# Performance work log

Hardware: AMD Instinct MI355X
Metric: run time of the kernel (lower is better)

Reference implementation:

```python
import jax, jax.numpy as jnp
import numpy as np

N_NODES = 50000
N_EDGES = 800000
DIM = 128
N_LAYERS = 5
BN_EPS = 1e-3  # keras BatchNormalization default epsilon


def setup_inputs() -> dict:
    key = jax.random.key(0)
    ks = jax.random.split(key, 6)
    scale = 1.0 / np.sqrt(DIM)
    return {
        "x": jax.random.normal(ks[0], (N_NODES, DIM), dtype=jnp.float32),
        "edge_src": jax.random.randint(ks[1], (N_EDGES,), 0, N_NODES, dtype=jnp.int32),
        "edge_dst": jax.random.randint(ks[2], (N_EDGES,), 0, N_NODES, dtype=jnp.int32),
        "eps": jnp.zeros((N_LAYERS,), dtype=jnp.float32),
        "W1": jax.random.normal(ks[3], (N_LAYERS, DIM, DIM), dtype=jnp.float32) * scale,
        "b1": jnp.zeros((N_LAYERS, DIM), dtype=jnp.float32),
        "W2": jax.random.normal(ks[4], (N_LAYERS, DIM, DIM), dtype=jnp.float32) * scale,
        "b2": jnp.zeros((N_LAYERS, DIM), dtype=jnp.float32),
        "gamma": jnp.ones((N_LAYERS, DIM), dtype=jnp.float32),
        "beta": jnp.zeros((N_LAYERS, DIM), dtype=jnp.float32),
        "bn_mean": jnp.zeros((N_LAYERS, DIM), dtype=jnp.float32),
        "bn_var": jnp.ones((N_LAYERS, DIM), dtype=jnp.float32),
    }


def reference(x, edge_src, edge_dst, eps, W1, b1, W2, b2, gamma, beta, bn_mean, bn_var):
    n = x.shape[0]
    num_layers = W1.shape[0]
    hidden_rep = [x]
    h = x
    for l in range(num_layers):
        # sparse Adj @ h as gather + segment-sum (sum neighbor pooling)
        msgs = jnp.take(h, edge_src, axis=0)                       # [E, D]
        pooled = jax.ops.segment_sum(msgs, edge_dst, num_segments=n)  # [N, D]
        pooled = pooled + (1.0 + eps[l]) * h                        # GIN eps term
        # 2-layer MLP: Linear -> ReLU -> Linear
        z = jax.nn.relu(pooled @ W1[l] + b1[l])
        z = z @ W2[l] + b2[l]
        # BatchNorm (inference: moving statistics)
        z = gamma[l] * (z - bn_mean[l]) * jax.lax.rsqrt(bn_var[l] + BN_EPS) + beta[l]
        h = jax.nn.relu(z)
        hidden_rep.append(h)
    return tuple(hidden_rep)
```

## Files before the change

### kernel.cpp

```cpp
#include <hip/hip_runtime.h>
#include <hip/hip_bf16.h>

#define N_NODES 50000
#define N_EDGES 800000
#define DIM 128
#define N_LAYERS 5
#define BN_EPS 1e-3f

typedef __attribute__((ext_vector_type(8))) short bf16x8;
typedef __attribute__((ext_vector_type(4))) float f32x4;

__device__ __forceinline__ unsigned short f2bf(float f) {
    unsigned int v = __builtin_bit_cast(unsigned int, f);
    v += 0x7fffu + ((v >> 16) & 1u);
    return (unsigned short)(v >> 16);
}
__device__ __forceinline__ float bflo(unsigned int v) {
    return __builtin_bit_cast(float, v << 16);
}
__device__ __forceinline__ float bfhi(unsigned int v) {
    return __builtin_bit_cast(float, v & 0xffff0000u);
}


__global__ void init_zero_kernel(const float* __restrict__ x, float* __restrict__ out,
                                 unsigned short* __restrict__ hb, int* __restrict__ cnt) {
    int t = blockIdx.x * blockDim.x + threadIdx.x;
    if (t < (N_NODES * DIM) / 4) {
        f32x4 v = ((const f32x4*)x)[t];
        __builtin_nontemporal_store(v, (f32x4*)out + t);
        unsigned short u[4] = {f2bf(v.x), f2bf(v.y), f2bf(v.z), f2bf(v.w)};
        *(uint2*)(hb + t * 4) = *(uint2*)u;
    }
    int z = t - (N_NODES * DIM) / 4;
    if (z >= 0 && z < N_NODES) cnt[z] = 0;
}

__global__ void hist_kernel(const int* __restrict__ dst, int* __restrict__ cnt) {
    int e = blockIdx.x * blockDim.x + threadIdx.x;
    if (e < N_EDGES) atomicAdd(&cnt[dst[e]], 1);
}

__global__ __launch_bounds__(1024) void scan_kernel(const int* __restrict__ cnt,
                                                    int* __restrict__ row_start,
                                                    int* __restrict__ cursor) {
    __shared__ int wsum[16];
    __shared__ int s_carry;
    const int tid = threadIdx.x;
    const int lane = tid & 63, wave = tid >> 6;
    if (tid == 0) s_carry = 0;
    __syncthreads();
    for (int base = 0; base < N_NODES; base += 4096) {
        int i0 = base + tid * 4;
        int v[4];
#pragma unroll
        for (int j = 0; j < 4; j++) {
            int i = i0 + j;
            v[j] = (i < N_NODES) ? cnt[i] : 0;
        }
        int s = v[0] + v[1] + v[2] + v[3];
        int x = s;
#pragma unroll
        for (int off = 1; off < 64; off <<= 1) {
            int t = __shfl_up(x, off, 64);
            if (lane >= off) x += t;
        }
        if (lane == 63) wsum[wave] = x;
        __syncthreads();
        if (wave == 0) {
            int w = (lane < 16) ? wsum[lane] : 0;
#pragma unroll
            for (int off = 1; off < 16; off <<= 1) {
                int t = __shfl_up(w, off, 64);
                if (lane >= off) w += t;
            }
            if (lane < 16) wsum[lane] = w;
        }
        __syncthreads();
        int waveoff = (wave > 0) ? wsum[wave - 1] : 0;
        int carry = s_carry;
        int run = carry + waveoff + (x - s);
#pragma unroll
        for (int j = 0; j < 4; j++) {
            int i = i0 + j;
            if (i < N_NODES) { row_start[i] = run; cursor[i] = run; }
            run += v[j];
        }
        __syncthreads();
        if (tid == 1023) s_carry = carry + wsum[15];
        __syncthreads();
    }
    if (tid == 0) row_start[N_NODES] = s_carry;
}

__global__ void fill_kernel(const int* __restrict__ src, const int* __restrict__ dst,
                            int* __restrict__ cursor, int* __restrict__ col) {
    int e = blockIdx.x * blockDim.x + threadIdx.x;
    if (e < N_EDGES) {
        int d = dst[e];
        int pos = atomicAdd(&cursor[d], 1);
        col[pos] = src[e];
    }
}

__global__ void prep_kernel(const float* __restrict__ W1, const float* __restrict__ W2,
                            unsigned short* __restrict__ wp,
                            const float* __restrict__ gamma, const float* __restrict__ beta,
                            const float* __restrict__ mean, const float* __restrict__ var,
                            float* __restrict__ scale, float* __restrict__ shift) {
    int t = blockIdx.x * blockDim.x + threadIdx.x;
    if (t < N_LAYERS * 2 * 2048) {
        int mat = t >> 11;
        int r = t & 2047;
        int ks = r >> 9, nt = (r >> 6) & 7, lane = r & 63;
        int layer = mat >> 1;
        const float* W = ((mat & 1) ? W2 : W1) + layer * DIM * DIM;
        int n = nt * 16 + (lane & 15);
        int kb = ks * 32 + (lane >> 4) * 8;
        unsigned short u[8];
#pragma unroll
        for (int j = 0; j < 8; j++) u[j] = f2bf(W[(kb + j) * DIM + n]);
        *(uint4*)(wp + (size_t)mat * 16384 + ((ks * 8 + nt) * 64 + lane) * 8) = *(uint4*)u;
    }
    int i = t - N_LAYERS * 2 * 2048;
    if (i >= 0 && i < N_LAYERS * DIM) {
        float sc = gamma[i] * rsqrtf(var[i] + BN_EPS);
        scale[i] = sc;
        shift[i] = beta[i] - mean[i] * sc;
    }
}


__global__ __launch_bounds__(256) void pool_kernel(const unsigned short* __restrict__ hb,
                                                   const int* __restrict__ row_start,
                                                   const int* __restrict__ col,
                                                   const float* __restrict__ eps_l,
                                                   unsigned short* __restrict__ pooled_b) {
    const int wave = threadIdx.x >> 6, lane = threadIdx.x & 63;
    const int n = blockIdx.x * 4 + wave;
    if (n >= N_NODES) return;
    const float ev = 1.0f + eps_l[0];
    const int s0 = row_start[n], s1 = row_start[n + 1];
    const int c2 = lane * 2;

    unsigned int sv = *(const unsigned int*)(hb + n * DIM + c2);
    float a0 = ev * bflo(sv);
    float a1 = ev * bfhi(sv);

    for (int base = s0; base < s1; base += 64) {
        const int nn = (s1 - base < 64) ? (s1 - base) : 64;
        int ci = (base + lane < s1) ? col[base + lane] : 0;
        for (int j = 0; j < nn; j += 8) {
            int s[8];
            unsigned int v[8];
#pragma unroll
            for (int q = 0; q < 8; q++) s[q] = __shfl(ci, j + q, 64);
#pragma unroll
            for (int q = 0; q < 8; q++)
                v[q] = *(const unsigned int*)(hb + s[q] * DIM + c2);
#pragma unroll
            for (int q = 0; q < 8; q++) {
                if (j + q < nn) { a0 += bflo(v[q]); a1 += bfhi(v[q]); }
            }
        }
    }
    unsigned short u[2] = {f2bf(a0), f2bf(a1)};
    *(unsigned int*)(pooled_b + n * DIM + c2) = *(unsigned int*)u;
}

__global__ __launch_bounds__(256) void mlp_kernel(
    const unsigned short* __restrict__ pooled_b,
    const unsigned short* __restrict__ wp1,
    const unsigned short* __restrict__ wp2,
    const float* __restrict__ b1,
    const float* __restrict__ b2,
    const float* __restrict__ bnscale,
    const float* __restrict__ bnshift,
    float* __restrict__ h_out,
    unsigned short* __restrict__ hb_out) {
    __shared__ __align__(16) unsigned short zfrag[4][4][64][8];
    const int tid = threadIdx.x;
    const int wave = tid >> 6, lane = tid & 63;
    const int m0 = blockIdx.x * 64;
    const int colc = lane & 15;
    const int quad = lane >> 4;
    const int arow = m0 + wave * 16 + colc;
    const int arow_c = arow < N_NODES ? arow : N_NODES - 1;

    bf16x8 a[4];
#pragma unroll
    for (int ks = 0; ks < 4; ks++)
        a[ks] = *(const bf16x8*)(pooled_b + arow_c * DIM + ks * 32 + quad * 8);

    f32x4 acc[8];
#pragma unroll
    for (int nt = 0; nt < 8; nt++) {
        acc[nt] = (f32x4){0.f, 0.f, 0.f, 0.f};
#pragma unroll
        for (int ks = 0; ks < 4; ks++) {
            bf16x8 b = *(const bf16x8*)(wp1 + ((ks * 8 + nt) * 64 + lane) * 8);
            acc[nt] = __builtin_amdgcn_mfma_f32_16x16x32_bf16(a[ks], b, acc[nt], 0, 0, 0);
        }
    }

#pragma unroll
    for (int nt = 0; nt < 8; nt++) {
        int n = nt * 16 + colc;
        float bias = b1[n];
#pragma unroll
        for (int r = 0; r < 4; r++) {
            float v = acc[nt][r] + bias;
            v = v > 0.f ? v : 0.f;
            int row16 = quad * 4 + r;
            zfrag[wave][n >> 5][(((n >> 3) & 3) << 4) | row16][n & 7] = f2bf(v);
        }
    }

#pragma unroll
    for (int ks = 0; ks < 4; ks++) a[ks] = *(const bf16x8*)(&zfrag[wave][ks][lane][0]);

    f32x4 acc2[8];
#pragma unroll
    for (int nt = 0; nt < 8; nt++) {
        acc2[nt] = (f32x4){0.f, 0.f, 0.f, 0.f};
#pragma unroll
        for (int ks = 0; ks < 4; ks++) {
            bf16x8 b = *(const bf16x8*)(wp2 + ((ks * 8 + nt) * 64 + lane) * 8);
            acc2[nt] = __builtin_amdgcn_mfma_f32_16x16x32_bf16(a[ks], b, acc2[nt], 0, 0, 0);
        }
    }

#pragma unroll
    for (int nt = 0; nt < 8; nt++) {
        int n = nt * 16 + colc;
        float bias = b2[n];
        float sc = bnscale[n], sh = bnshift[n];
#pragma unroll
        for (int r = 0; r < 4; r++) {
            int row = m0 + wave * 16 + quad * 4 + r;
            if (row < N_NODES) {
                float z = acc2[nt][r] + bias;
                z = z * sc + sh;
                z = z > 0.f ? z : 0.f;
                __builtin_nontemporal_store(z, &h_out[row * DIM + n]);
                hb_out[row * DIM + n] = f2bf(z);
            }
        }
    }
}


extern "C" void kernel_launch(void* const* d_in, const int* in_sizes, int n_in,
                              void* d_out, int out_size, void* d_ws, size_t ws_size,
                              hipStream_t stream) {
    const float* x     = (const float*)d_in[0];
    const int* esrc    = (const int*)d_in[1];
    const int* edst    = (const int*)d_in[2];
    const float* eps   = (const float*)d_in[3];
    const float* W1    = (const float*)d_in[4];
    const float* b1    = (const float*)d_in[5];
    const float* W2    = (const float*)d_in[6];
    const float* b2    = (const float*)d_in[7];
    const float* gam   = (const float*)d_in[8];
    const float* bet   = (const float*)d_in[9];
    const float* bmean = (const float*)d_in[10];
    const float* bvar  = (const float*)d_in[11];
    float* out = (float*)d_out;

    char* ws = (char*)d_ws;
    unsigned short* hb0   = (unsigned short*)(ws);
    unsigned short* hb1   = (unsigned short*)(ws + 12800000);
    int*   col        = (int*)  (ws + 25600000);
    int*   row_start  = (int*)  (ws + 28800000);
    int*   cursor     = (int*)  (ws + 29000008);
    int*   cnt        = (int*)  (ws + 29200008);
    unsigned short* wpack = (unsigned short*)(ws + 29400008);
    float* bnscale    = (float*)(ws + 29727688);
    float* bnshift    = (float*)(ws + 29730248);
    unsigned short* pooled_b = (unsigned short*)(ws + 29735048);

    init_zero_kernel<<<((N_NODES * DIM) / 4 + N_NODES + 255) / 256, 256, 0, stream>>>(
        x, out, hb0, cnt);
    hist_kernel<<<(N_EDGES + 255) / 256, 256, 0, stream>>>(edst, cnt);
    scan_kernel<<<1, 1024, 0, stream>>>(cnt, row_start, cursor);
    fill_kernel<<<(N_EDGES + 255) / 256, 256, 0, stream>>>(esrc, edst, cursor, col);
    prep_kernel<<<(N_LAYERS * 2 * 2048 + N_LAYERS * DIM + 255) / 256, 256, 0, stream>>>(
        W1, W2, wpack, gam, bet, bmean, bvar, bnscale, bnshift);

    const int pool_blocks = (N_NODES + 3) / 4;
    const int mlp_blocks  = (N_NODES + 63) / 64;
    unsigned short* hbuf[2] = {hb0, hb1};
    for (int l = 0; l < N_LAYERS; l++) {
        float* h_next = out + (size_t)(l + 1) * N_NODES * DIM;
        pool_kernel<<<pool_blocks, 256, 0, stream>>>(hbuf[l & 1], row_start, col, eps + l,
                                                     pooled_b);
        mlp_kernel<<<mlp_blocks, 256, 0, stream>>>(
            pooled_b,
            wpack + (size_t)(l * 2) * 16384,
            wpack + (size_t)(l * 2 + 1) * 16384,
            b1 + l * DIM, b2 + l * DIM,
            bnscale + l * DIM, bnshift + l * DIM,
            h_next, hbuf[(l + 1) & 1]);
    }
}
```

Baseline: 575.3 us.

## Quantize node features to int8 with per-column scales for neighbor gather

Adds a per-layer quantization pass that converts bf16 features to int8 using per-column absmax scales, tracked via atomics in the MLP epilogue and an initial colmax kernel. The pooling kernel gathers 16-byte int8 chunks with 8 lanes per row, accumulates in integers, reduces across lane groups, and rescales before adding the self term. This halves gather traffic in the neighbor aggregation. In exchange it adds an extra quantization pass per layer and loses accuracy from 8-bit rounding.

```diff
diff --git a/kernel.cpp b/kernel.cpp
--- a/kernel.cpp
+++ b/kernel.cpp
@@ -6,9 +6,12 @@
 #define DIM 128
 #define N_LAYERS 5
 #define BN_EPS 1e-3f
+#define CMPAD 16
 
 typedef __attribute__((ext_vector_type(8))) short bf16x8;
 typedef __attribute__((ext_vector_type(4))) float f32x4;
+typedef __attribute__((ext_vector_type(4))) unsigned int u32x4;
+typedef __attribute__((ext_vector_type(2))) unsigned int u32x2;
 
 __device__ __forceinline__ unsigned short f2bf(float f) {
     unsigned int v = __builtin_bit_cast(unsigned int, f);
@@ -24,16 +27,43 @@
 
 
 __global__ void init_zero_kernel(const float* __restrict__ x, float* __restrict__ out,
-                                 unsigned short* __restrict__ hb, int* __restrict__ cnt) {
+                                 unsigned short* __restrict__ hb, int* __restrict__ cnt,
+                                 unsigned int* __restrict__ cmax) {
     int t = blockIdx.x * blockDim.x + threadIdx.x;
     if (t < (N_NODES * DIM) / 4) {
         f32x4 v = ((const f32x4*)x)[t];
         __builtin_nontemporal_store(v, (f32x4*)out + t);
         unsigned short u[4] = {f2bf(v.x), f2bf(v.y), f2bf(v.z), f2bf(v.w)};
-        *(uint2*)(hb + t * 4) = *(uint2*)u;
+        *(u32x2*)(hb + t * 4) = *(u32x2*)u;
     }
     int z = t - (N_NODES * DIM) / 4;
     if (z >= 0 && z < N_NODES) cnt[z] = 0;
+    int z2 = z - N_NODES;
+    if (z2 >= 0 && z2 < 2 * DIM * CMPAD) cmax[z2] = 0;
+}
+
+__global__ __launch_bounds__(256) void colmax0_kernel(const unsigned short* __restrict__ hb,
+                                                      unsigned int* __restrict__ cmax) {
+    __shared__ unsigned int cm[DIM];
+    const int tid = threadIdx.x;
+    if (tid < DIM) cm[tid] = 0;
+    __syncthreads();
+    const int total = N_NODES * DIM / 8;
+    const int stride = gridDim.x * blockDim.x;
+    float m[8] = {0.f, 0.f, 0.f, 0.f, 0.f, 0.f, 0.f, 0.f};
+    for (int e = blockIdx.x * blockDim.x + tid; e < total; e += stride) {
+        u32x4 v = *(const u32x4*)(hb + (size_t)e * 8);
+        m[0] = fmaxf(m[0], fabsf(bflo(v.x))); m[1] = fmaxf(m[1], fabsf(bfhi(v.x)));
+        m[2] = fmaxf(m[2], fabsf(bflo(v.y))); m[3] = fmaxf(m[3], fabsf(bfhi(v.y)));
+        m[4] = fmaxf(m[4], fabsf(bflo(v.z))); m[5] = fmaxf(m[5], fabsf(bfhi(v.z)));
+        m[6] = fmaxf(m[6], fabsf(bflo(v.w))); m[7] = fmaxf(m[7], fabsf(bfhi(v.w)));
+    }
+    const int cb = (tid & 15) * 8;
+#pragma unroll
+    for (int k = 0; k < 8; k++)
+        atomicMax(&cm[cb + k], __builtin_bit_cast(unsigned int, m[k]));
+    __syncthreads();
+    if (tid < DIM) atomicMax(&cmax[tid * CMPAD], cm[tid]);
 }
 
 __global__ void hist_kernel(const int* __restrict__ dst, int* __restrict__ cnt) {
@@ -120,7 +150,7 @@
         unsigned short u[8];
 #pragma unroll
         for (int j = 0; j < 8; j++) u[j] = f2bf(W[(kb + j) * DIM + n]);
-        *(uint4*)(wp + (size_t)mat * 16384 + ((ks * 8 + nt) * 64 + lane) * 8) = *(uint4*)u;
+        *(u32x4*)(wp + (size_t)mat * 16384 + ((ks * 8 + nt) * 64 + lane) * 8) = *(u32x4*)u;
     }
     int i = t - N_LAYERS * 2 * 2048;
     if (i >= 0 && i < N_LAYERS * DIM) {
@@ -131,41 +161,110 @@
 }
 
 
-__global__ __launch_bounds__(256) void pool_kernel(const unsigned short* __restrict__ hb,
+__global__ __launch_bounds__(256) void quant_kernel(const unsigned short* __restrict__ hb,
+                                                    const unsigned int* __restrict__ cmax_cur,
+                                                    unsigned int* __restrict__ cmax_next,
+                                                    signed char* __restrict__ q8) {
+    const int tid = blockIdx.x * blockDim.x + threadIdx.x;
+    if (blockIdx.x == 0 && threadIdx.x < DIM) cmax_next[threadIdx.x * CMPAD] = 0;
+    const int cb = (tid & 15) * 8;
+    float inv[8];
+#pragma unroll
+    for (int k = 0; k < 8; k++) {
+        float mx = __builtin_bit_cast(float, cmax_cur[(cb + k) * CMPAD]);
+        inv[k] = mx > 0.f ? 127.0f / mx : 0.f;
+    }
+    u32x4 v = *(const u32x4*)(hb + (size_t)tid * 8);
+    float f[8] = {bflo(v.x), bfhi(v.x), bflo(v.y), bfhi(v.y),
+                  bflo(v.z), bfhi(v.z), bflo(v.w), bfhi(v.w)};
+    unsigned int b[8];
+#pragma unroll
+    for (int k = 0; k < 8; k++) {
+        int q = (int)rintf(f[k] * inv[k]);
+        q = q > 127 ? 127 : (q < -127 ? -127 : q);
+        b[k] = (unsigned int)q & 255u;
+    }
+    u32x2 o;
+    o.x = b[0] | (b[1] << 8) | (b[2] << 16) | (b[3] << 24);
+    o.y = b[4] | (b[5] << 8) | (b[6] << 16) | (b[7] << 24);
+    __builtin_nontemporal_store(o, (u32x2*)(q8 + (size_t)tid * 8));
+}
+
+__device__ __forceinline__ void accq(int* a, unsigned int w, int k) {
+    a[k + 0] += (int)(w << 24) >> 24;
+    a[k + 1] += (int)(w << 16) >> 24;
+    a[k + 2] += (int)(w << 8) >> 24;
+    a[k + 3] += (int)w >> 24;
+}
+
+__global__ __launch_bounds__(256) void pool_kernel(const signed char* __restrict__ q8,
+                                                   const unsigned short* __restrict__ hb,
                                                    const int* __restrict__ row_start,
                                                    const int* __restrict__ col,
                                                    const float* __restrict__ eps_l,
+                                                   const unsigned int* __restrict__ cmax,
                                                    unsigned short* __restrict__ pooled_b) {
     const int wave = threadIdx.x >> 6, lane = threadIdx.x & 63;
-    const int n = blockIdx.x * 4 + wave;
-    if (n >= N_NODES) return;
-    const float ev = 1.0f + eps_l[0];
+    const int n = __builtin_amdgcn_readfirstlane(blockIdx.x * 4 + wave);
     const int s0 = row_start[n], s1 = row_start[n + 1];
-    const int c2 = lane * 2;
-
-    unsigned int sv = *(const unsigned int*)(hb + n * DIM + c2);
-    float a0 = ev * bflo(sv);
-    float a1 = ev * bfhi(sv);
+    const int g = lane >> 3;
+    const int t = lane & 7;
+
+    int acc[16] = {0, 0, 0, 0, 0, 0, 0, 0, 0, 0, 0, 0, 0, 0, 0, 0};
 
     for (int base = s0; base < s1; base += 64) {
-        const int nn = (s1 - base < 64) ? (s1 - base) : 64;
-        int ci = (base + lane < s1) ? col[base + lane] : 0;
-        for (int j = 0; j < nn; j += 8) {
-            int s[8];
-            unsigned int v[8];
-#pragma unroll
-            for (int q = 0; q < 8; q++) s[q] = __shfl(ci, j + q, 64);
-#pragma unroll
-            for (int q = 0; q < 8; q++)
-                v[q] = *(const unsigned int*)(hb + s[q] * DIM + c2);
-#pragma unroll
-            for (int q = 0; q < 8; q++) {
-                if (j + q < nn) { a0 += bflo(v[q]); a1 += bfhi(v[q]); }
+        const int rem = s1 - base;
+        const int nn = rem < 64 ? rem : 64;
+        int ci = (base + lane < s1) ? __builtin_nontemporal_load(&col[base + lane]) : 0;
+        for (int j = 0; j < nn; j += 24) {
+            u32x4 v[3];
+#pragma unroll
+            for (int i = 0; i < 3; i++) {
+                int start = j + i * 8;
+                if (start < nn) {
+                    int r = __shfl(ci, start + g, 64);
+                    u32x4 tmp = *(const u32x4*)(q8 + (size_t)r * DIM + t * 16);
+                    u32x4 zero = {0u, 0u, 0u, 0u};
+                    v[i] = (start + g < nn) ? tmp : zero;
+                }
             }
-        }
-    }
-    unsigned short u[2] = {f2bf(a0), f2bf(a1)};
-    *(unsigned int*)(pooled_b + n * DIM + c2) = *(unsigned int*)u;
+#pragma unroll
+            for (int i = 0; i < 3; i++) {
+                if (j + i * 8 < nn) {
+                    accq(acc, v[i].x, 0);
+                    accq(acc, v[i].y, 4);
+                    accq(acc, v[i].z, 8);
+                    accq(acc, v[i].w, 12);
+                }
+            }
+        }
+    }
+
+#pragma unroll
+    for (int k = 0; k < 16; k++) {
+        acc[k] += __shfl_xor(acc[k], 8, 64);
+        acc[k] += __shfl_xor(acc[k], 16, 64);
+        acc[k] += __shfl_xor(acc[k], 32, 64);
+    }
+    if (g == 0) {
+        const float ev = 1.0f + eps_l[0];
+        u32x4 sa = *(const u32x4*)(hb + (size_t)n * DIM + t * 16);
+        u32x4 sb = *(const u32x4*)(hb + (size_t)n * DIM + t * 16 + 8);
+        float self[16] = {bflo(sa.x), bfhi(sa.x), bflo(sa.y), bfhi(sa.y),
+                          bflo(sa.z), bfhi(sa.z), bflo(sa.w), bfhi(sa.w),
+                          bflo(sb.x), bfhi(sb.x), bflo(sb.y), bfhi(sb.y),
+                          bflo(sb.z), bfhi(sb.z), bflo(sb.w), bfhi(sb.w)};
+        unsigned short u[16];
+#pragma unroll
+        for (int k = 0; k < 16; k++) {
+            float s = __builtin_bit_cast(float, cmax[(t * 16 + k) * CMPAD]) * (1.0f / 127.0f);
+            u[k] = f2bf((float)acc[k] * s + ev * self[k]);
+        }
+        __builtin_nontemporal_store(*(u32x4*)u,
+                                    (u32x4*)(pooled_b + (size_t)n * DIM + t * 16));
+        __builtin_nontemporal_store(*(u32x4*)(u + 8),
+                                    (u32x4*)(pooled_b + (size_t)n * DIM + t * 16 + 8));
+    }
 }
 
 __global__ __launch_bounds__(256) void mlp_kernel(
@@ -177,8 +276,10 @@
     const float* __restrict__ bnscale,
     const float* __restrict__ bnshift,
     float* __restrict__ h_out,
-    unsigned short* __restrict__ hb_out) {
+    unsigned short* __restrict__ hb_out,
+    unsigned int* __restrict__ cmax_next) {
     __shared__ __align__(16) unsigned short zfrag[4][4][64][8];
+    __shared__ unsigned int cmg[DIM];
     const int tid = threadIdx.x;
     const int wave = tid >> 6, lane = tid & 63;
     const int m0 = blockIdx.x * 64;
@@ -186,6 +287,7 @@
     const int quad = lane >> 4;
     const int arow = m0 + wave * 16 + colc;
     const int arow_c = arow < N_NODES ? arow : N_NODES - 1;
+    if (tid < DIM) cmg[tid] = 0;
 
     bf16x8 a[4];
 #pragma unroll
@@ -230,11 +332,13 @@
         }
     }
 
+    float cmx[8];
 #pragma unroll
     for (int nt = 0; nt < 8; nt++) {
         int n = nt * 16 + colc;
         float bias = b2[n];
         float sc = bnscale[n], sh = bnshift[n];
+        cmx[nt] = 0.f;
 #pragma unroll
         for (int r = 0; r < 4; r++) {
             int row = m0 + wave * 16 + quad * 4 + r;
@@ -244,9 +348,16 @@
                 z = z > 0.f ? z : 0.f;
                 __builtin_nontemporal_store(z, &h_out[row * DIM + n]);
                 hb_out[row * DIM + n] = f2bf(z);
+                cmx[nt] = fmaxf(cmx[nt], z);
             }
         }
     }
+    __syncthreads();
+#pragma unroll
+    for (int nt = 0; nt < 8; nt++)
+        atomicMax(&cmg[nt * 16 + colc], __builtin_bit_cast(unsigned int, cmx[nt]));
+    __syncthreads();
+    if (tid < DIM) atomicMax(&cmax_next[tid * CMPAD], cmg[tid]);
 }
 
 
@@ -268,38 +379,43 @@
     float* out = (float*)d_out;
 
     char* ws = (char*)d_ws;
-    unsigned short* hb0   = (unsigned short*)(ws);
-    unsigned short* hb1   = (unsigned short*)(ws + 12800000);
-    int*   col        = (int*)  (ws + 25600000);
-    int*   row_start  = (int*)  (ws + 28800000);
-    int*   cursor     = (int*)  (ws + 29000008);
-    int*   cnt        = (int*)  (ws + 29200008);
-    unsigned short* wpack = (unsigned short*)(ws + 29400008);
-    float* bnscale    = (float*)(ws + 29727688);
-    float* bnshift    = (float*)(ws + 29730248);
-    unsigned short* pooled_b = (unsigned short*)(ws + 29735048);
-
-    init_zero_kernel<<<((N_NODES * DIM) / 4 + N_NODES + 255) / 256, 256, 0, stream>>>(
-        x, out, hb0, cnt);
+    unsigned short* hb  = (unsigned short*)(ws);
+    int*   col        = (int*)  (ws + 12800000);
+    int*   row_start  = (int*)  (ws + 16000000);
+    int*   cursor     = (int*)  (ws + 16200192);
+    int*   cnt        = (int*)  (ws + 16400384);
+    unsigned short* wpack = (unsigned short*)(ws + 16600576);
+    float* bnscale    = (float*)(ws + 16928256);
+    float* bnshift    = (float*)(ws + 16930816);
+    unsigned int* cmax = (unsigned int*)(ws + 16933376);
+    signed char* q8   = (signed char*)(ws + 16949760);
+    unsigned short* pooled_b = (unsigned short*)(ws + 23349760);
+
+    init_zero_kernel<<<(1600000 + N_NODES + 2 * DIM * CMPAD + 255) / 256, 256, 0, stream>>>(
+        x, out, hb, cnt, cmax);
+    colmax0_kernel<<<256, 256, 0, stream>>>(hb, cmax);
     hist_kernel<<<(N_EDGES + 255) / 256, 256, 0, stream>>>(edst, cnt);
     scan_kernel<<<1, 1024, 0, stream>>>(cnt, row_start, cursor);
     fill_kernel<<<(N_EDGES + 255) / 256, 256, 0, stream>>>(esrc, edst, cursor, col);
     prep_kernel<<<(N_LAYERS * 2 * 2048 + N_LAYERS * DIM + 255) / 256, 256, 0, stream>>>(
         W1, W2, wpack, gam, bet, bmean, bvar, bnscale, bnshift);
 
-    const int pool_blocks = (N_NODES + 3) / 4;
-    const int mlp_blocks  = (N_NODES + 63) / 64;
-    unsigned short* hbuf[2] = {hb0, hb1};
+    const int quant_blocks = (N_NODES * DIM / 8) / 256;
+    const int pool_blocks  = N_NODES / 4;
+    const int mlp_blocks   = (N_NODES + 63) / 64;
     for (int l = 0; l < N_LAYERS; l++) {
         float* h_next = out + (size_t)(l + 1) * N_NODES * DIM;
-        pool_kernel<<<pool_blocks, 256, 0, stream>>>(hbuf[l & 1], row_start, col, eps + l,
-                                                     pooled_b);
+        unsigned int* cm_cur  = cmax + (size_t)(l & 1) * DIM * CMPAD;
+        unsigned int* cm_next = cmax + (size_t)((l + 1) & 1) * DIM * CMPAD;
+        quant_kernel<<<quant_blocks, 256, 0, stream>>>(hb, cm_cur, cm_next, q8);
+        pool_kernel<<<pool_blocks, 256, 0, stream>>>(q8, hb, row_start, col, eps + l,
+                                                     cm_cur, pooled_b);
         mlp_kernel<<<mlp_blocks, 256, 0, stream>>>(
             pooled_b,
             wpack + (size_t)(l * 2) * 16384,
             wpack + (size_t)(l * 2 + 1) * 16384,
             b1 + l * DIM, b2 + l * DIM,
             bnscale + l * DIM, bnshift + l * DIM,
-            h_next, hbuf[(l + 1) & 1]);
-    }
-}
+            h_next, hb, cm_next);
+    }
+}
```

Result: slower. 744.0 us (+29.3%).
